# Optimization experiments

Hardware: AMD Instinct MI355X
Metric: run time of the kernel (lower is better)

The kernel has to match this reference:

```python
import jax, jax.numpy as jnp
import numpy as np

B, S, F, K = 64, 1024, 128, 64  # batch, seq(=l), feat(=d), bottleneck k


def setup_inputs() -> dict:
    key = jax.random.key(0)
    ks = jax.random.split(key, 24)
    r = lambda k_, sh, s=0.05: (jax.random.normal(k_, sh, dtype=jnp.float32) * s)
    inp = {
        'f1_norm': jax.random.normal(ks[0], (B, S, F), dtype=jnp.float32),
        'f2_norm': jax.random.normal(ks[1], (B, S, F), dtype=jnp.float32),
        'f3_norm': jax.random.normal(ks[2], (B, S, F), dtype=jnp.float32),
        # AMLP params (Linear(F, 2F))
        'Wi': r(ks[3], (2 * F, F)), 'bi': r(ks[4], (2 * F,)),
        'Wq': r(ks[5], (2 * F, F)), 'bq': r(ks[6], (2 * F,)),
        'Wvp': r(ks[7], (2 * F, F)), 'bvp': r(ks[8], (2 * F,)),
        # affine_{a,v,l}: Linear(l, l, bias=False) -> weight [l, l]
        'Aa': r(ks[9], (S, S)), 'Av': r(ks[10], (S, S)), 'Al': r(ks[11], (S, S)),
        # W_{a,v,t}: Linear(l, k) -> [k, l]
        'Wa': r(ks[12], (K, S)), 'Wv': r(ks[13], (K, S)), 'Wt': r(ks[14], (K, S)),
        # W_c{a,v,t}: Linear(2d, k) -> [k, 2F]
        'Wca': r(ks[15], (K, 2 * F)), 'Wcv': r(ks[16], (K, 2 * F)), 'Wct': r(ks[17], (K, 2 * F)),
        # W_h{a,v,t}: Linear(k, l) -> [l, k]
        'Wha': r(ks[18], (S, K)), 'Whv': r(ks[19], (S, K)), 'Wht': r(ks[20], (S, K)),
    }
    return inp


def _amlp(txt, aud, vis, Wi, bi, Wq, bq, Wvp, bvp):
    f1 = jnp.einsum('bsf,gf->bsg', txt, Wi) + bi  # [B,S,2F]
    f2 = jnp.einsum('bsf,gf->bsg', aud, Wq) + bq
    f3 = jnp.einsum('bsf,gf->bsg', vis, Wvp) + bvp
    n1 = jnp.linalg.norm(f1)
    n2 = jnp.linalg.norm(f2)
    n3 = jnp.linalg.norm(f3)
    # faithful to source: third term is scalar factor3 * norm3 (broadcast)
    exp_out = (n1 / (n1 + n2)) * f1 + (n2 / (n1 + n2)) * f2 + (n3 / (n1 + n2 + n3)) * n3
    b, s, g = exp_out.shape
    z = exp_out.reshape(b, s, g // 2, 2).sum(-1)  # AvgPool1d(2,2) * 2 == pair sum
    # F.normalize default dim=1 (over sequence axis for 3D tensor)
    z = z / jnp.maximum(jnp.linalg.norm(z, axis=1, keepdims=True), 1e-12)
    return z  # [B,S,F]


def reference(f1_norm, f2_norm, f3_norm, Wi, bi, Wq, bq, Wvp, bvp,
              Aa, Av, Al, Wa, Wv, Wt, Wca, Wcv, Wct, Wha, Whv, Wht):
    txt, aud, vis = f1_norm, f2_norm, f3_norm
    G = _amlp(txt, aud, vis, Wi, bi, Wq, bq, Wvp, bvp)  # [B,S,F]

    G_ag = jnp.concatenate([aud, G], axis=-1)  # [B,S,2F]
    G_vg = jnp.concatenate([vis, G], axis=-1)
    G_lg = jnp.concatenate([txt, G], axis=-1)
    scale = np.sqrt(G_ag.shape[-1]).astype(np.float32)  # sqrt(2F); same for all three

    # a_j = affine(G_xg^T); att = x^T @ a_j^T  ==  x^T @ (A @ G_xg)
    AGa = jnp.einsum('ts,bsc->btc', Aa, G_ag)
    C_a = jnp.tanh(jnp.einsum('bsf,bsc->bfc', aud, AGa) / scale)  # [B,F,2F]
    AGv = jnp.einsum('ts,bsc->btc', Av, G_ag)  # NOTE: source bug uses G_ag, not G_vg
    C_v = jnp.tanh(jnp.einsum('bsf,bsc->bfc', vis, AGv) / scale)
    AGl = jnp.einsum('ts,bsc->btc', Al, G_lg)
    C_t = jnp.tanh(jnp.einsum('bsf,bsc->bfc', txt, AGl) / scale)

    H_a = jax.nn.relu(jnp.einsum('bfc,kc->bfk', C_a, Wca) + jnp.einsum('bsf,ks->bfk', aud, Wa))
    H_v = jax.nn.relu(jnp.einsum('bfc,kc->bfk', C_v, Wcv) + jnp.einsum('bsf,ks->bfk', vis, Wv))
    H_t = jax.nn.relu(jnp.einsum('bfc,kc->bfk', C_t, Wct) + jnp.einsum('bsf,ks->bfk', txt, Wt))

    out_a = jnp.einsum('bfk,sk->bsf', H_a, Wha) + aud  # [B,S,F]
    out_v = jnp.einsum('bfk,sk->bsf', H_v, Whv) + vis
    out_t = jnp.einsum('bfk,sk->bsf', H_t, Wht) + txt
    return (out_t, out_a, out_v)
```

## Files before the change

kernel.cpp:

```cpp
#include <hip/hip_runtime.h>
#include <math.h>

constexpr int Bb = 64;
constexpr int Ss = 1024;
constexpr int Ff = 128;
constexpr int G2 = 256;
constexpr int Kk = 64;
constexpr int NE = 1152;

typedef __bf16 bfrag __attribute__((ext_vector_type(8)));
typedef float  facc  __attribute__((ext_vector_type(4)));
typedef short  s8v   __attribute__((ext_vector_type(8)));

__device__ __forceinline__ short f2bfs(float f) {
  union { float f; unsigned u; } v; v.f = f;
  unsigned r = v.u + 0x7FFFu + ((v.u >> 16) & 1u);
  return (short)(r >> 16);
}
__device__ __forceinline__ float bf2fs(short s) {
  union { unsigned u; float f; } v; v.u = ((unsigned)(unsigned short)s) << 16;
  return v.f;
}
__device__ __forceinline__ facc mfma16(bfrag a, bfrag b, facc c) {
  return __builtin_amdgcn_mfma_f32_16x16x32_bf16(a, b, c, 0, 0, 0);
}
__device__ __forceinline__ void gld16(const void* g, void* l) {
  __builtin_amdgcn_global_load_lds(
      (const __attribute__((address_space(1))) void*)g,
      (__attribute__((address_space(3))) void*)l, 16, 0, 0);
}

__global__ void k_transpose(const float* __restrict__ aud, const float* __restrict__ vis,
                            const float* __restrict__ txt, short* __restrict__ xT) {
  __shared__ float tile[64][65];
  int z = blockIdx.z;
  int mod = z >> 6, b = z & 63;
  const float* x = (mod == 0) ? aud : (mod == 1) ? vis : txt;
  int s0 = blockIdx.x * 64, f0 = blockIdx.y * 64;
  int tid = threadIdx.x;
  for (int i = 0; i < 16; ++i) {
    int idx = i * 256 + tid;
    int si = idx >> 6, fi = idx & 63;
    tile[si][fi] = x[((size_t)b * Ss + s0 + si) * Ff + f0 + fi];
  }
  __syncthreads();
  short* dst = xT + ((size_t)mod * Bb + b) * Ff * Ss;
  for (int i = 0; i < 16; ++i) {
    int idx = i * 256 + tid;
    int fi = idx >> 6, si = idx & 63;
    dst[(size_t)(f0 + fi) * Ss + s0 + si] = f2bfs(tile[si][fi]);
  }
}

__global__ void k_build_aextT(const float* __restrict__ Aa, const float* __restrict__ Av,
                              const float* __restrict__ Al, const float* __restrict__ Wa,
                              const float* __restrict__ Wv, const float* __restrict__ Wt,
                              short* __restrict__ aextT) {
  __shared__ float tile[64][65];
  int mod = blockIdx.z;
  const float* A = (mod == 0) ? Aa : (mod == 1) ? Av : Al;
  const float* W = (mod == 0) ? Wa : (mod == 1) ? Wv : Wt;
  short* dst = aextT + (size_t)mod * NE * Ss;
  int n0 = blockIdx.x * 64, t0 = blockIdx.y * 64;
  int tid = threadIdx.x;
  if (n0 < Ss) {
    for (int i = 0; i < 16; ++i) {
      int idx = i * 256 + tid;
      int ti = idx >> 6, nj = idx & 63;
      tile[ti][nj] = A[(size_t)(t0 + ti) * Ss + n0 + nj];
    }
    __syncthreads();
    for (int i = 0; i < 16; ++i) {
      int idx = i * 256 + tid;
      int nj = idx >> 6, ti = idx & 63;
      dst[(size_t)(n0 + nj) * Ss + t0 + ti] = f2bfs(tile[ti][nj]);
    }
  } else if (n0 < Ss + Kk) {
    for (int i = 0; i < 16; ++i) {
      int idx = i * 256 + tid;
      int j = idx >> 6, tt = idx & 63;
      dst[(size_t)(n0 + j) * Ss + t0 + tt] = f2bfs(W[(size_t)(n0 - Ss + j) * Ss + t0 + tt]);
    }
  } else {
    for (int i = 0; i < 16; ++i) {
      int idx = i * 256 + tid;
      int j = idx >> 6, tt = idx & 63;
      dst[(size_t)(n0 + j) * Ss + t0 + tt] = 0;
    }
  }
}

__global__ void k_build_w(const float* __restrict__ Wca, const float* __restrict__ Wcv,
                          const float* __restrict__ Wct, const float* __restrict__ Wha,
                          const float* __restrict__ Whv, const float* __restrict__ Wht,
                          const float* __restrict__ Wi, const float* __restrict__ Wq,
                          const float* __restrict__ Wvp,
                          short* __restrict__ wcb, short* __restrict__ whb,
                          short* __restrict__ wbar) {
  int idx = blockIdx.x * 256 + threadIdx.x;
  const int n1 = 3 * Kk * G2;
  const int n2 = n1 + 3 * Ss * Kk;
  if (idx < n1) {
    int mod = idx / (Kk * G2), r = idx - mod * (Kk * G2);
    const float* W = (mod == 0) ? Wca : (mod == 1) ? Wcv : Wct;
    wcb[idx] = f2bfs(W[r]);
  } else if (idx < n2) {
    int j = idx - n1;
    int mod = j / (Ss * Kk), r = j - mod * (Ss * Kk);
    const float* W = (mod == 0) ? Wha : (mod == 1) ? Whv : Wht;
    whb[j] = f2bfs(W[r]);
  } else {
    int j = idx - n2;
    int mod = j / (G2 * Ff), r = j - mod * (G2 * Ff);
    int n = r >> 7, k = r & 127;
    const float* W = (mod == 0) ? Wi : (mod == 1) ? Wq : Wvp;
    wbar[mod * G2 * Ff + (((k >> 3) * G2 + n) * 8) + (k & 7)] = f2bfs(W[r]);
  }
}

__global__ void __launch_bounds__(256) k_amlp(
    const float* __restrict__ txt, const float* __restrict__ aud, const float* __restrict__ vis,
    const float* __restrict__ bi, const float* __restrict__ bq, const float* __restrict__ bvp,
    const short* __restrict__ wbar,
    short* __restrict__ p1, short* __restrict__ p2, float* __restrict__ sumsq) {
  int mod = blockIdx.y;
  const float* x    = (mod == 0) ? txt : (mod == 1) ? aud : vis;
  const float* bias = (mod == 0) ? bi  : (mod == 1) ? bq  : bvp;
  const short* wbm  = wbar + mod * G2 * Ff;
  short* pout = (mod == 0) ? p1 : (mod == 1) ? p2 : nullptr;

  __shared__ short wlds[G2 * Ff];
  __shared__ float wred[4];
  int tid = threadIdx.x, lane = tid & 63, wave = tid >> 6;
  int quad = lane >> 4, nl = lane & 15;
  for (int i = 0; i < 16; ++i) {
    int o = (i * 256 + tid) * 8;
    gld16(wbm + o, wlds + o);
  }
  __syncthreads();

  float bia[16];
  for (int t = 0; t < 16; ++t) bia[t] = bias[t * 16 + nl];

  facc zero = {0.f, 0.f, 0.f, 0.f};
  float sq = 0.f;
  for (int rg = 0; rg < 4; ++rg) {
    int arow = blockIdx.x * 256 + rg * 64 + wave * 16 + nl;
    const float* xrow = x + (size_t)arow * Ff;
    facc acc[16];
    for (int t = 0; t < 16; ++t) acc[t] = zero;
    for (int k0 = 0; k0 < Ff; k0 += 32) {
      float4 a0 = *(const float4*)(xrow + k0 + quad * 8);
      float4 a1 = *(const float4*)(xrow + k0 + quad * 8 + 4);
      bfrag af;
      af[0]=(__bf16)a0.x; af[1]=(__bf16)a0.y; af[2]=(__bf16)a0.z; af[3]=(__bf16)a0.w;
      af[4]=(__bf16)a1.x; af[5]=(__bf16)a1.y; af[6]=(__bf16)a1.z; af[7]=(__bf16)a1.w;
      int chunk = (k0 >> 3) + quad;
      for (int t = 0; t < 16; ++t) {
        bfrag bfr = *(const bfrag*)(wlds + ((size_t)chunk * G2 + t * 16 + nl) * 8);
        acc[t] = mfma16(af, bfr, acc[t]);
      }
    }
    int drow = blockIdx.x * 256 + rg * 64 + wave * 16 + quad * 4;
    for (int t = 0; t < 16; ++t) {
      for (int r = 0; r < 4; ++r) {
        float fv = acc[t][r] + bia[t];
        sq += fv * fv;
        if (pout) {
          float fo = fv + __shfl_xor(fv, 1, 64);
          if ((lane & 1) == 0)
            pout[(size_t)(drow + r) * Ff + t * 8 + (nl >> 1)] = f2bfs(fo);
        }
      }
    }
  }
  for (int off = 32; off > 0; off >>= 1) sq += __shfl_down(sq, off, 64);
  if (lane == 0) wred[wave] = sq;
  __syncthreads();
  if (tid == 0) atomicAdd(&sumsq[mod], wred[0] + wred[1] + wred[2] + wred[3]);
}

__global__ void k_colnorm(const short* __restrict__ p1, const short* __restrict__ p2,
                          const float* __restrict__ sumsq, float* __restrict__ colnsq) {
  float n1 = sqrtf(sumsq[0]), n2 = sqrtf(sumsq[1]), n3 = sqrtf(sumsq[2]);
  float w1 = n1 / (n1 + n2), w2 = n2 / (n1 + n2);
  float tc = 2.f * n3 * n3 / (n1 + n2 + n3);
  int b = blockIdx.x, j = threadIdx.x;
  int s0 = blockIdx.y * 64;
  float a = 0.f;
  for (int s = s0; s < s0 + 64; ++s) {
    size_t off = ((size_t)b * Ss + s) * Ff + j;
    float z = w1 * bf2fs(p1[off]) + w2 * bf2fs(p2[off]) + tc;
    a += z * z;
  }
  atomicAdd(&colnsq[b * Ff + j], a);
}

__global__ void k_gnormT(const short* __restrict__ p1, const short* __restrict__ p2,
                         const float* __restrict__ sumsq, const float* __restrict__ colnsq,
                         short* __restrict__ gT) {
  __shared__ float tile[64][65];
  float n1 = sqrtf(sumsq[0]), n2 = sqrtf(sumsq[1]), n3 = sqrtf(sumsq[2]);
  float w1 = n1 / (n1 + n2), w2 = n2 / (n1 + n2);
  float tc = 2.f * n3 * n3 / (n1 + n2 + n3);
  int b = blockIdx.z, s0 = blockIdx.x * 64, f0 = blockIdx.y * 64;
  int tid = threadIdx.x;
  for (int i = 0; i < 16; ++i) {
    int idx = i * 256 + tid;
    int si = idx >> 6, fi = idx & 63;
    size_t off = ((size_t)b * Ss + s0 + si) * Ff + f0 + fi;
    float z = w1 * bf2fs(p1[off]) + w2 * bf2fs(p2[off]) + tc;
    float cn = fmaxf(sqrtf(colnsq[b * Ff + f0 + fi]), 1e-12f);
    tile[si][fi] = z / cn;
  }
  __syncthreads();
  short* dst = gT + (size_t)b * Ff * Ss;
  for (int i = 0; i < 16; ++i) {
    int idx = i * 256 + tid;
    int fi = idx >> 6, si = idx & 63;
    dst[(size_t)(f0 + fi) * Ss + s0 + si] = f2bfs(tile[si][fi]);
  }
}

__global__ void __launch_bounds__(256) k_mgemm(const short* __restrict__ xT,
                                               const short* __restrict__ aextT,
                                               short* __restrict__ mxext) {
  int mod = blockIdx.z;
  const short* Ap = xT + (size_t)mod * Bb * Ff * Ss;
  const short* Bp = aextT + (size_t)mod * NE * Ss;
  short* Op = mxext + (size_t)mod * Bb * Ff * NE;
  int M0 = blockIdx.x * 128, N0 = blockIdx.y * 128;
  __shared__ short As[128 * 32];
  __shared__ short Bs[128 * 32];
  int tid = threadIdx.x, lane = tid & 63, wave = tid >> 6;
  int quad = lane >> 4, nl = lane & 15;
  int wm = (wave >> 1) * 64, wn = (wave & 1) * 64;
  int r0 = tid >> 2, c8 = (tid & 3) * 8;
  facc zero = {0.f, 0.f, 0.f, 0.f};
  facc acc[4][4];
  for (int i = 0; i < 4; ++i) for (int j = 0; j < 4; ++j) acc[i][j] = zero;
  for (int k0 = 0; k0 < Ss; k0 += 32) {
    __syncthreads();
    gld16(Ap + (size_t)(M0 + r0) * Ss + k0 + c8,      As + tid * 8);
    gld16(Ap + (size_t)(M0 + 64 + r0) * Ss + k0 + c8, As + 2048 + tid * 8);
    gld16(Bp + (size_t)(N0 + r0) * Ss + k0 + c8,      Bs + tid * 8);
    gld16(Bp + (size_t)(N0 + 64 + r0) * Ss + k0 + c8, Bs + 2048 + tid * 8);
    __syncthreads();
    bfrag a[4], bfr[4];
    for (int mt = 0; mt < 4; ++mt)
      a[mt] = *(const bfrag*)(As + (wm + mt * 16 + nl) * 32 + quad * 8);
    for (int nt = 0; nt < 4; ++nt)
      bfr[nt] = *(const bfrag*)(Bs + (wn + nt * 16 + nl) * 32 + quad * 8);
    for (int mt = 0; mt < 4; ++mt)
      for (int nt = 0; nt < 4; ++nt)
        acc[mt][nt] = mfma16(a[mt], bfr[nt], acc[mt][nt]);
  }
  for (int mt = 0; mt < 4; ++mt)
    for (int nt = 0; nt < 4; ++nt)
      for (int r = 0; r < 4; ++r) {
        int row = M0 + wm + mt * 16 + quad * 4 + r;
        int col = N0 + wn + nt * 16 + nl;
        Op[(size_t)row * NE + col] = f2bfs(acc[mt][nt][r]);
      }
}

__global__ void __launch_bounds__(256) k_cgemm(const short* __restrict__ mxext,
                                               const short* __restrict__ xT,
                                               const short* __restrict__ gT,
                                               short* __restrict__ cc) {
  int b = blockIdx.x, nt4 = blockIdx.y, mod = blockIdx.z;
  const short* Ap = mxext + ((size_t)mod * Bb + b) * Ff * NE;
  const short* Bsrc = (nt4 < 2)
      ? (xT + (size_t)((mod == 2) ? 2 : 0) * Bb * Ff * Ss + (size_t)b * Ff * Ss
             + (size_t)(nt4 & 1) * 64 * Ss)
      : (gT + (size_t)b * Ff * Ss + (size_t)(nt4 & 1) * 64 * Ss);
  short* Cp = cc + ((size_t)mod * Bb + b) * Ff * G2;
  int ncol0 = nt4 * 64;
  __shared__ short As[128 * 32];
  __shared__ short Bs[64 * 32];
  int tid = threadIdx.x, lane = tid & 63, wave = tid >> 6;
  int quad = lane >> 4, nl = lane & 15;
  int wm = (wave >> 1) * 64, wn = (wave & 1) * 32;
  int r0 = tid >> 2, c8 = (tid & 3) * 8;
  facc zero = {0.f, 0.f, 0.f, 0.f};
  facc acc[4][2];
  for (int i = 0; i < 4; ++i) for (int j = 0; j < 2; ++j) acc[i][j] = zero;
  for (int k0 = 0; k0 < Ss; k0 += 32) {
    __syncthreads();
    gld16(Ap + (size_t)r0 * NE + k0 + c8,        As + tid * 8);
    gld16(Ap + (size_t)(64 + r0) * NE + k0 + c8, As + 2048 + tid * 8);
    gld16(Bsrc + (size_t)r0 * Ss + k0 + c8,      Bs + tid * 8);
    __syncthreads();
    bfrag a[4], bfr[2];
    for (int mt = 0; mt < 4; ++mt)
      a[mt] = *(const bfrag*)(As + (wm + mt * 16 + nl) * 32 + quad * 8);
    for (int nt = 0; nt < 2; ++nt)
      bfr[nt] = *(const bfrag*)(Bs + (wn + nt * 16 + nl) * 32 + quad * 8);
    for (int mt = 0; mt < 4; ++mt)
      for (int nt = 0; nt < 2; ++nt)
        acc[mt][nt] = mfma16(a[mt], bfr[nt], acc[mt][nt]);
  }
  for (int mt = 0; mt < 4; ++mt)
    for (int nt = 0; nt < 2; ++nt)
      for (int r = 0; r < 4; ++r) {
        int row = wm + mt * 16 + quad * 4 + r;
        int col = ncol0 + wn + nt * 16 + nl;
        Cp[(size_t)row * G2 + col] = f2bfs(tanhf(acc[mt][nt][r] * 0.0625f));
      }
}

__global__ void k_hgemm(const short* __restrict__ cc, const short* __restrict__ wcb,
                        const short* __restrict__ mxext, short* __restrict__ h) {
  int b = blockIdx.x, mod = blockIdx.y;
  const short* Cp = cc + ((size_t)mod * Bb + b) * Ff * G2;
  const short* Wp = wcb + (size_t)mod * Kk * G2;
  const short* T2 = mxext + ((size_t)mod * Bb + b) * Ff * NE + Ss;
  short* Hp = h + ((size_t)mod * Bb + b) * Ff * Kk;
  int tid = threadIdx.x, lane = tid & 63, wave = tid >> 6;
  int quad = lane >> 4, nl = lane & 15;
  facc zero = {0.f, 0.f, 0.f, 0.f};
  facc acc[2][4];
  for (int i = 0; i < 2; ++i) for (int j = 0; j < 4; ++j) acc[i][j] = zero;
  for (int k0 = 0; k0 < G2; k0 += 32) {
    bfrag a[2], bfr[4];
    for (int mt = 0; mt < 2; ++mt)
      a[mt] = *(const bfrag*)(Cp + (size_t)(wave * 32 + mt * 16 + nl) * G2 + k0 + quad * 8);
    for (int nt = 0; nt < 4; ++nt)
      bfr[nt] = *(const bfrag*)(Wp + (size_t)(nt * 16 + nl) * G2 + k0 + quad * 8);
    for (int mt = 0; mt < 2; ++mt)
      for (int nt = 0; nt < 4; ++nt)
        acc[mt][nt] = mfma16(a[mt], bfr[nt], acc[mt][nt]);
  }
  for (int mt = 0; mt < 2; ++mt)
    for (int nt = 0; nt < 4; ++nt)
      for (int r = 0; r < 4; ++r) {
        int row = wave * 32 + mt * 16 + quad * 4 + r;
        int col = nt * 16 + nl;
        float v = acc[mt][nt][r] + bf2fs(T2[(size_t)row * NE + col]);
        Hp[(size_t)row * Kk + col] = f2bfs(fmaxf(v, 0.f));
      }
}

__global__ void k_outgemm(const short* __restrict__ whb, const short* __restrict__ h,
                          const float* __restrict__ txt, const float* __restrict__ aud,
                          const float* __restrict__ vis, float* __restrict__ outp) {
  int s0 = blockIdx.x * 128, b = blockIdx.y, mod = blockIdx.z;
  const short* Wp = whb + (size_t)mod * Ss * Kk;
  const short* Hp = h + ((size_t)mod * Bb + b) * Ff * Kk;
  const float* xres = ((mod == 0) ? aud : (mod == 1) ? vis : txt) + (size_t)b * Ss * Ff;
  int slot = (mod == 0) ? 1 : (mod == 1) ? 2 : 0;
  float* Op = outp + ((size_t)slot * Bb + b) * Ss * Ff;
  int tid = threadIdx.x, lane = tid & 63, wave = tid >> 6;
  int quad = lane >> 4, nl = lane & 15;
  int wm = (wave >> 1) * 64, wn = (wave & 1) * 64;
  facc zero = {0.f, 0.f, 0.f, 0.f};
  facc acc[4][4];
  for (int i = 0; i < 4; ++i) for (int j = 0; j < 4; ++j) acc[i][j] = zero;
  for (int k0 = 0; k0 < Kk; k0 += 32) {
    bfrag a[4], bfr[4];
    for (int mt = 0; mt < 4; ++mt)
      a[mt] = *(const bfrag*)(Wp + (size_t)(s0 + wm + mt * 16 + nl) * Kk + k0 + quad * 8);
    for (int nt = 0; nt < 4; ++nt)
      bfr[nt] = *(const bfrag*)(Hp + (size_t)(wn + nt * 16 + nl) * Kk + k0 + quad * 8);
    for (int mt = 0; mt < 4; ++mt)
      for (int nt = 0; nt < 4; ++nt)
        acc[mt][nt] = mfma16(a[mt], bfr[nt], acc[mt][nt]);
  }
  for (int mt = 0; mt < 4; ++mt)
    for (int nt = 0; nt < 4; ++nt)
      for (int r = 0; r < 4; ++r) {
        int srow = s0 + wm + mt * 16 + quad * 4 + r;
        int col = wn + nt * 16 + nl;
        size_t o = (size_t)srow * Ff + col;
        Op[o] = acc[mt][nt][r] + xres[o];
      }
}

extern "C" void kernel_launch(void* const* d_in, const int* in_sizes, int n_in,
                              void* d_out, int out_size, void* d_ws, size_t ws_size,
                              hipStream_t stream) {
  const float* txt = (const float*)d_in[0];
  const float* aud = (const float*)d_in[1];
  const float* vis = (const float*)d_in[2];
  const float* Wi  = (const float*)d_in[3];
  const float* bi  = (const float*)d_in[4];
  const float* Wq  = (const float*)d_in[5];
  const float* bq  = (const float*)d_in[6];
  const float* Wvp = (const float*)d_in[7];
  const float* bvp = (const float*)d_in[8];
  const float* Aa  = (const float*)d_in[9];
  const float* Av  = (const float*)d_in[10];
  const float* Al  = (const float*)d_in[11];
  const float* Wa  = (const float*)d_in[12];
  const float* Wv  = (const float*)d_in[13];
  const float* Wt  = (const float*)d_in[14];
  const float* Wca = (const float*)d_in[15];
  const float* Wcv = (const float*)d_in[16];
  const float* Wct = (const float*)d_in[17];
  const float* Wha = (const float*)d_in[18];
  const float* Whv = (const float*)d_in[19];
  const float* Wht = (const float*)d_in[20];

  char* w = (char*)d_ws;
  float* sumsq  = (float*)w;
  float* colnsq = (float*)(w + 256);
  size_t off = 65536;
  short* xT    = (short*)(w + off); off += (size_t)3 * Bb * Ff * Ss * 2;
  short* aextT = (short*)(w + off); off += (size_t)3 * NE * Ss * 2;
  short* gT    = (short*)(w + off); off += (size_t)Bb * Ff * Ss * 2;
  short* mx    = (short*)(w + off);
  short* p1    = mx;
  short* p2    = mx + (size_t)Bb * Ss * Ff;
  off += (size_t)3 * Bb * Ff * NE * 2;
  short* cc    = (short*)(w + off); off += (size_t)3 * Bb * Ff * G2 * 2;
  short* h     = (short*)(w + off); off += (size_t)3 * Bb * Ff * Kk * 2;
  short* wcb   = (short*)(w + off); off += (size_t)3 * Kk * G2 * 2;
  short* whb   = (short*)(w + off); off += (size_t)3 * Ss * Kk * 2;
  short* wbar  = (short*)(w + off); off += (size_t)3 * G2 * Ff * 2;

  hipMemsetAsync(d_ws, 0, 65536, stream);
  k_transpose<<<dim3(16, 2, 192), 256, 0, stream>>>(aud, vis, txt, xT);
  k_build_aextT<<<dim3(NE / 64, 16, 3), 256, 0, stream>>>(Aa, Av, Al, Wa, Wv, Wt, aextT);
  k_build_w<<<(3 * Kk * G2 + 3 * Ss * Kk + 3 * G2 * Ff) / 256, 256, 0, stream>>>(
      Wca, Wcv, Wct, Wha, Whv, Wht, Wi, Wq, Wvp, wcb, whb, wbar);
  k_amlp<<<dim3(Bb * Ss / 256, 3), 256, 0, stream>>>(txt, aud, vis, bi, bq, bvp,
                                                     wbar, p1, p2, sumsq);
  k_colnorm<<<dim3(Bb, 16), 128, 0, stream>>>(p1, p2, sumsq, colnsq);
  k_gnormT<<<dim3(16, 2, Bb), 256, 0, stream>>>(p1, p2, sumsq, colnsq, gT);
  k_mgemm<<<dim3(Bb * Ff / 128, NE / 128, 3), 256, 0, stream>>>(xT, aextT, mx);
  k_cgemm<<<dim3(Bb, 4, 3), 256, 0, stream>>>(mx, xT, gT, cc);
  k_hgemm<<<dim3(Bb, 3), 256, 0, stream>>>(cc, wcb, mx, h);
  k_outgemm<<<dim3(Ss / 128, Bb, 3), 256, 0, stream>>>(whb, h, txt, aud, vis, (float*)d_out);
}
```

Before: 478.2 us.

## Fuse C and H GEMMs and swizzle LDS with deeper K tiles in mgemm

Merges the tanh C-GEMM and the H-GEMM into one 512-thread kernel per (batch, modality), keeping the C tile in LDS instead of writing it to global memory. The M-GEMM and the fused kernel move to 64-wide K tiles with XOR-swizzled shared memory, which halves barrier count and avoids LDS bank conflicts. The fused kernel launches far fewer blocks and needs a larger LDS allocation, which lowers parallelism for that stage.

New measurement: 471.3 us. No clear change (-1.4%).

```diff
diff --git a/kernel.cpp b/kernel.cpp
--- a/kernel.cpp
+++ b/kernel.cpp
@@ -230,30 +230,39 @@
   const short* Bp = aextT + (size_t)mod * NE * Ss;
   short* Op = mxext + (size_t)mod * Bb * Ff * NE;
   int M0 = blockIdx.x * 128, N0 = blockIdx.y * 128;
-  __shared__ short As[128 * 32];
-  __shared__ short Bs[128 * 32];
+  __shared__ short As[128 * 64];
+  __shared__ short Bs[128 * 64];
   int tid = threadIdx.x, lane = tid & 63, wave = tid >> 6;
   int quad = lane >> 4, nl = lane & 15;
   int wm = (wave >> 1) * 64, wn = (wave & 1) * 64;
-  int r0 = tid >> 2, c8 = (tid & 3) * 8;
   facc zero = {0.f, 0.f, 0.f, 0.f};
   facc acc[4][4];
   for (int i = 0; i < 4; ++i) for (int j = 0; j < 4; ++j) acc[i][j] = zero;
-  for (int k0 = 0; k0 < Ss; k0 += 32) {
+  for (int k0 = 0; k0 < Ss; k0 += 64) {
     __syncthreads();
-    gld16(Ap + (size_t)(M0 + r0) * Ss + k0 + c8,      As + tid * 8);
-    gld16(Ap + (size_t)(M0 + 64 + r0) * Ss + k0 + c8, As + 2048 + tid * 8);
-    gld16(Bp + (size_t)(N0 + r0) * Ss + k0 + c8,      Bs + tid * 8);
-    gld16(Bp + (size_t)(N0 + 64 + r0) * Ss + k0 + c8, Bs + 2048 + tid * 8);
+#pragma unroll
+    for (int i = 0; i < 4; ++i) {
+      int idx = i * 256 + tid;
+      int r = idx >> 3, cs = ((idx & 7) ^ (r & 7)) * 8;
+      gld16(Ap + (size_t)(M0 + r) * Ss + k0 + cs, As + idx * 8);
+      gld16(Bp + (size_t)(N0 + r) * Ss + k0 + cs, Bs + idx * 8);
+    }
     __syncthreads();
-    bfrag a[4], bfr[4];
-    for (int mt = 0; mt < 4; ++mt)
-      a[mt] = *(const bfrag*)(As + (wm + mt * 16 + nl) * 32 + quad * 8);
-    for (int nt = 0; nt < 4; ++nt)
-      bfr[nt] = *(const bfrag*)(Bs + (wn + nt * 16 + nl) * 32 + quad * 8);
-    for (int mt = 0; mt < 4; ++mt)
-      for (int nt = 0; nt < 4; ++nt)
-        acc[mt][nt] = mfma16(a[mt], bfr[nt], acc[mt][nt]);
+#pragma unroll
+    for (int kc = 0; kc < 2; ++kc) {
+      bfrag a[4], bfr[4];
+      for (int mt = 0; mt < 4; ++mt) {
+        int row = wm + mt * 16 + nl;
+        a[mt] = *(const bfrag*)(As + row * 64 + (((kc * 4 + quad) ^ (row & 7)) * 8));
+      }
+      for (int nt = 0; nt < 4; ++nt) {
+        int row = wn + nt * 16 + nl;
+        bfr[nt] = *(const bfrag*)(Bs + row * 64 + (((kc * 4 + quad) ^ (row & 7)) * 8));
+      }
+      for (int mt = 0; mt < 4; ++mt)
+        for (int nt = 0; nt < 4; ++nt)
+          acc[mt][nt] = mfma16(a[mt], bfr[nt], acc[mt][nt]);
+    }
   }
   for (int mt = 0; mt < 4; ++mt)
     for (int nt = 0; nt < 4; ++nt)
@@ -264,81 +273,86 @@
       }
 }
 
-__global__ void __launch_bounds__(256) k_cgemm(const short* __restrict__ mxext,
-                                               const short* __restrict__ xT,
-                                               const short* __restrict__ gT,
-                                               short* __restrict__ cc) {
-  int b = blockIdx.x, nt4 = blockIdx.y, mod = blockIdx.z;
+__global__ void __launch_bounds__(512) k_chgemm(const short* __restrict__ mxext,
+                                                const short* __restrict__ xT,
+                                                const short* __restrict__ gT,
+                                                const short* __restrict__ wcb,
+                                                short* __restrict__ h) {
+  int b = blockIdx.x, mod = blockIdx.y;
   const short* Ap = mxext + ((size_t)mod * Bb + b) * Ff * NE;
-  const short* Bsrc = (nt4 < 2)
-      ? (xT + (size_t)((mod == 2) ? 2 : 0) * Bb * Ff * Ss + (size_t)b * Ff * Ss
-             + (size_t)(nt4 & 1) * 64 * Ss)
-      : (gT + (size_t)b * Ff * Ss + (size_t)(nt4 & 1) * 64 * Ss);
-  short* Cp = cc + ((size_t)mod * Bb + b) * Ff * G2;
-  int ncol0 = nt4 * 64;
-  __shared__ short As[128 * 32];
-  __shared__ short Bs[64 * 32];
+  const short* xTb = xT + (size_t)((mod == 2) ? 2 : 0) * Bb * Ff * Ss + (size_t)b * Ff * Ss;
+  const short* gTb = gT + (size_t)b * Ff * Ss;
+  const short* Wp = wcb + (size_t)mod * Kk * G2;
+  short* Hp = h + ((size_t)mod * Bb + b) * Ff * Kk;
+
+  __shared__ short smem[128 * 272];
+  short* As = smem;
+  short* Bs = smem + 128 * 64;
+
   int tid = threadIdx.x, lane = tid & 63, wave = tid >> 6;
   int quad = lane >> 4, nl = lane & 15;
-  int wm = (wave >> 1) * 64, wn = (wave & 1) * 32;
-  int r0 = tid >> 2, c8 = (tid & 3) * 8;
+  int wm = (wave >> 2) * 64, wn = (wave & 3) * 64;
   facc zero = {0.f, 0.f, 0.f, 0.f};
-  facc acc[4][2];
-  for (int i = 0; i < 4; ++i) for (int j = 0; j < 2; ++j) acc[i][j] = zero;
-  for (int k0 = 0; k0 < Ss; k0 += 32) {
+  facc acc[4][4];
+  for (int i = 0; i < 4; ++i) for (int j = 0; j < 4; ++j) acc[i][j] = zero;
+  for (int k0 = 0; k0 < Ss; k0 += 64) {
     __syncthreads();
-    gld16(Ap + (size_t)r0 * NE + k0 + c8,        As + tid * 8);
-    gld16(Ap + (size_t)(64 + r0) * NE + k0 + c8, As + 2048 + tid * 8);
-    gld16(Bsrc + (size_t)r0 * Ss + k0 + c8,      Bs + tid * 8);
+#pragma unroll
+    for (int i = 0; i < 2; ++i) {
+      int idx = i * 512 + tid;
+      int r = idx >> 3, cs = ((idx & 7) ^ (r & 7)) * 8;
+      gld16(Ap + (size_t)r * NE + k0 + cs, As + idx * 8);
+    }
+#pragma unroll
+    for (int i = 0; i < 4; ++i) {
+      int idx = i * 512 + tid;
+      int r = idx >> 3, cs = ((idx & 7) ^ (r & 7)) * 8;
+      const short* src = (r < 128) ? (xTb + (size_t)r * Ss) : (gTb + (size_t)(r - 128) * Ss);
+      gld16(src + k0 + cs, Bs + idx * 8);
+    }
     __syncthreads();
-    bfrag a[4], bfr[2];
-    for (int mt = 0; mt < 4; ++mt)
-      a[mt] = *(const bfrag*)(As + (wm + mt * 16 + nl) * 32 + quad * 8);
-    for (int nt = 0; nt < 2; ++nt)
-      bfr[nt] = *(const bfrag*)(Bs + (wn + nt * 16 + nl) * 32 + quad * 8);
-    for (int mt = 0; mt < 4; ++mt)
-      for (int nt = 0; nt < 2; ++nt)
-        acc[mt][nt] = mfma16(a[mt], bfr[nt], acc[mt][nt]);
-  }
+#pragma unroll
+    for (int kc = 0; kc < 2; ++kc) {
+      bfrag a[4], bfr[4];
+      for (int mt = 0; mt < 4; ++mt) {
+        int row = wm + mt * 16 + nl;
+        a[mt] = *(const bfrag*)(As + row * 64 + (((kc * 4 + quad) ^ (row & 7)) * 8));
+      }
+      for (int nt = 0; nt < 4; ++nt) {
+        int row = wn + nt * 16 + nl;
+        bfr[nt] = *(const bfrag*)(Bs + row * 64 + (((kc * 4 + quad) ^ (row & 7)) * 8));
+      }
+      for (int mt = 0; mt < 4; ++mt)
+        for (int nt = 0; nt < 4; ++nt)
+          acc[mt][nt] = mfma16(a[mt], bfr[nt], acc[mt][nt]);
+    }
+  }
+  __syncthreads();
+  short* Cs = smem;
   for (int mt = 0; mt < 4; ++mt)
-    for (int nt = 0; nt < 2; ++nt)
+    for (int nt = 0; nt < 4; ++nt)
       for (int r = 0; r < 4; ++r) {
         int row = wm + mt * 16 + quad * 4 + r;
-        int col = ncol0 + wn + nt * 16 + nl;
-        Cp[(size_t)row * G2 + col] = f2bfs(tanhf(acc[mt][nt][r] * 0.0625f));
-      }
-}
-
-__global__ void k_hgemm(const short* __restrict__ cc, const short* __restrict__ wcb,
-                        const short* __restrict__ mxext, short* __restrict__ h) {
-  int b = blockIdx.x, mod = blockIdx.y;
-  const short* Cp = cc + ((size_t)mod * Bb + b) * Ff * G2;
-  const short* Wp = wcb + (size_t)mod * Kk * G2;
-  const short* T2 = mxext + ((size_t)mod * Bb + b) * Ff * NE + Ss;
-  short* Hp = h + ((size_t)mod * Bb + b) * Ff * Kk;
-  int tid = threadIdx.x, lane = tid & 63, wave = tid >> 6;
-  int quad = lane >> 4, nl = lane & 15;
-  facc zero = {0.f, 0.f, 0.f, 0.f};
-  facc acc[2][4];
-  for (int i = 0; i < 2; ++i) for (int j = 0; j < 4; ++j) acc[i][j] = zero;
+        int col = wn + nt * 16 + nl;
+        Cs[row * 272 + col] = f2bfs(tanhf(acc[mt][nt][r] * 0.0625f));
+      }
+  __syncthreads();
+  facc hacc[4];
+  for (int nt = 0; nt < 4; ++nt) hacc[nt] = zero;
   for (int k0 = 0; k0 < G2; k0 += 32) {
-    bfrag a[2], bfr[4];
-    for (int mt = 0; mt < 2; ++mt)
-      a[mt] = *(const bfrag*)(Cp + (size_t)(wave * 32 + mt * 16 + nl) * G2 + k0 + quad * 8);
-    for (int nt = 0; nt < 4; ++nt)
-      bfr[nt] = *(const bfrag*)(Wp + (size_t)(nt * 16 + nl) * G2 + k0 + quad * 8);
-    for (int mt = 0; mt < 2; ++mt)
-      for (int nt = 0; nt < 4; ++nt)
-        acc[mt][nt] = mfma16(a[mt], bfr[nt], acc[mt][nt]);
-  }
-  for (int mt = 0; mt < 2; ++mt)
-    for (int nt = 0; nt < 4; ++nt)
-      for (int r = 0; r < 4; ++r) {
-        int row = wave * 32 + mt * 16 + quad * 4 + r;
-        int col = nt * 16 + nl;
-        float v = acc[mt][nt][r] + bf2fs(T2[(size_t)row * NE + col]);
-        Hp[(size_t)row * Kk + col] = f2bfs(fmaxf(v, 0.f));
-      }
+    bfrag ca = *(const bfrag*)(Cs + (wave * 16 + nl) * 272 + k0 + quad * 8);
+    for (int nt = 0; nt < 4; ++nt) {
+      bfrag wb = *(const bfrag*)(Wp + (size_t)(nt * 16 + nl) * G2 + k0 + quad * 8);
+      hacc[nt] = mfma16(ca, wb, hacc[nt]);
+    }
+  }
+  for (int nt = 0; nt < 4; ++nt)
+    for (int r = 0; r < 4; ++r) {
+      int row = wave * 16 + quad * 4 + r;
+      int col = nt * 16 + nl;
+      float v = hacc[nt][r] + bf2fs(Ap[(size_t)row * NE + Ss + col]);
+      Hp[(size_t)row * Kk + col] = f2bfs(fmaxf(v, 0.f));
+    }
 }
 
 __global__ void k_outgemm(const short* __restrict__ whb, const short* __restrict__ h,
@@ -412,7 +426,6 @@
   short* p1    = mx;
   short* p2    = mx + (size_t)Bb * Ss * Ff;
   off += (size_t)3 * Bb * Ff * NE * 2;
-  short* cc    = (short*)(w + off); off += (size_t)3 * Bb * Ff * G2 * 2;
   short* h     = (short*)(w + off); off += (size_t)3 * Bb * Ff * Kk * 2;
   short* wcb   = (short*)(w + off); off += (size_t)3 * Kk * G2 * 2;
   short* whb   = (short*)(w + off); off += (size_t)3 * Ss * Kk * 2;
@@ -428,7 +441,6 @@
   k_colnorm<<<dim3(Bb, 16), 128, 0, stream>>>(p1, p2, sumsq, colnsq);
   k_gnormT<<<dim3(16, 2, Bb), 256, 0, stream>>>(p1, p2, sumsq, colnsq, gT);
   k_mgemm<<<dim3(Bb * Ff / 128, NE / 128, 3), 256, 0, stream>>>(xT, aextT, mx);
-  k_cgemm<<<dim3(Bb, 4, 3), 256, 0, stream>>>(mx, xT, gT, cc);
-  k_hgemm<<<dim3(Bb, 3), 256, 0, stream>>>(cc, wcb, mx, h);
+  k_chgemm<<<dim3(Bb, 3), 512, 0, stream>>>(mx, xT, gT, wcb, h);
   k_outgemm<<<dim3(Ss / 128, Bb, 3), 256, 0, stream>>>(whb, h, txt, aud, vis, (float*)d_out);
 }
```
